# Performance work log

Hardware: AMD Instinct MI355X
Metric: run time of the kernel (lower is better)

The kernel has to match this reference:

```python
import jax, jax.numpy as jnp
import numpy as np

B, C, D, T = 64, 512, 32, 32
DT = D * T
K = 128            # valid_num: top-K proposals kept for NMS-style pooling
MARGIN = 0.2       # opt.global_margin
MAX_VIOLATION = True
EPS = 1e-8         # torch.cosine_similarity eps


def _l2n(x, axis):
    # torch cosine_similarity normalizes each vector by max(||x||, eps)
    return x / jnp.maximum(jnp.linalg.norm(x, axis=axis, keepdims=True), EPS)


def _cos(a, b, axis):
    return jnp.sum(_l2n(a, axis) * _l2n(b, axis), axis=axis)


def setup_inputs() -> dict:
    key = jax.random.key(0)
    k1, k2, k3 = jax.random.split(key, 3)
    videos = jax.random.normal(k1, (B, C, D, T), jnp.float32)
    sentences = jax.random.normal(k2, (B, C), jnp.float32)
    iou = jax.random.uniform(k3, (DT, DT), jnp.float32)
    iou_maps = 0.5 * (iou + iou.T)
    iou_maps = iou_maps.at[jnp.arange(DT), jnp.arange(DT)].set(1.0)
    mask = jnp.ones((D, T), jnp.float32)
    lam = jnp.asarray(0.125, jnp.float32)
    return {"videos": videos, "sentences": sentences, "lam": lam,
            "mask": mask, "valid_num": K, "iou_maps": iou_maps}


def reference(videos, sentences, lam, mask, valid_num, iou_maps):
    b, c, d, t = videos.shape
    dt = d * t
    # center over channel dim (dim=1 in torch)
    V = videos - jnp.mean(videos, axis=1, keepdims=True)          # [b,c,d,t]
    S = sentences - jnp.mean(sentences, axis=1, keepdims=True)    # [b,c]
    Vf = V.reshape(b, c, dt)
    Vn = _l2n(Vf, axis=1)                                         # unit over c
    Sn = _l2n(S, axis=1)
    mflat = mask.reshape(dt)

    # cosine sim of every sentence vs every video proposal: [b_sent, b_vid, dt]
    cross = jnp.einsum('ic,jcp->ijp', Sn, Vn)
    cross = jnp.where(mflat == 0, -jnp.inf, cross)

    # --- per-sample positive pooling (loop 1) ---
    self_score = cross[jnp.arange(b), jnp.arange(b)]              # [b, dt]
    w = jax.nn.softmax(self_score, axis=-1)
    video_pos = jnp.einsum('bp,bcp->bc', w, Vf)                   # [b, c]

    # sentence-sentence sims + hard negative mining
    sim = Sn @ Sn.T                                               # [b, b]
    idx = jnp.argsort(-sim, axis=1)                               # descending
    neg_idx = idx[:, 6:b - 5]                                     # b > 11 path
    neg_sents = S[neg_idx]                                        # [b, b-11, c]
    pos_score = _cos(video_pos, S, axis=1)                        # [b]
    neg_score = _cos(video_pos[:, None, :], neg_sents, axis=2)    # [b, b-11]
    vas_loss = jnp.mean(jax.nn.relu(MARGIN + neg_score - pos_score[:, None]), axis=1).mean()

    # cross-video pseudo-positive (crov), gated on nearest-neighbor sim > 0.9
    nn_idx = idx[:, 1]
    pse = Vf[nn_idx]                                              # [b, c, dt]
    vsim = jax.nn.softmax(_cos(video_pos[:, :, None], pse, axis=1), axis=-1)  # [b, dt]
    p_v = jnp.einsum('bp,bcp->bc', vsim, pse)
    n_v = jnp.einsum('bp,bcp->bc', (1.0 - vsim) * mflat, pse) / (valid_num - 1)
    crov = jax.nn.relu(MARGIN + _cos(video_pos, n_v, axis=1) - _cos(video_pos, p_v, axis=1))
    gate = sim[jnp.arange(b), nn_idx] > 0.9
    crov_loss = jnp.where(gate, crov, 0.0).mean()

    # --- NMS-weighted video score pooling (loop 2) ---
    pmap = self_score.reshape(b, d, t)                            # postive_map
    topv, topi = jax.lax.top_k(cross, valid_num)                  # [b,b,K]
    # pairwise IoU among the top-K proposals of each (sentence, video) pair
    iou = iou_maps[topi[..., :, None], topi[..., None, :]]        # [b,b,K,K]
    lower = jnp.tril(jnp.ones((valid_num, valid_num), bool), -1)  # l < k
    decay = jnp.prod(1.0 - jnp.where(lower, iou, 0.0), axis=-1)   # [b,b,K]
    wk = jax.nn.softmax(lam * topv, axis=-1)
    scores = jnp.sum(wk * decay * topv, axis=-1)                  # [b,b]

    # bidirectional margin ranking loss
    diag = jnp.diag(scores)[:, None]
    eye = jnp.eye(b, dtype=bool)
    cost_s = jnp.where(eye, 0.0, jax.nn.relu(MARGIN + scores - diag))
    cost_im = jnp.where(eye, 0.0, jax.nn.relu(MARGIN + scores - diag.T))
    if MAX_VIOLATION:
        cost_s = cost_s.max(axis=1)
        cost_im = cost_im.max(axis=0)
    loss = cost_s.sum() / b + cost_im.sum() / b + vas_loss + crov_loss
    return loss, pmap
```

## Files before the change

kernel.cpp:

```cpp
#include <hip/hip_runtime.h>
#include <hip/hip_fp16.h>
#include <math.h>

#define BB 64
#define CC 512
#define DTT 1024
#define NNEG 53
#define MARGIN_ 0.2f
#define EPSV 1e-8f
#define LDB 132

typedef short s16x8 __attribute__((ext_vector_type(8)));
typedef float f32x4 __attribute__((ext_vector_type(4)));

__device__ __forceinline__ float bred_sum(float v, float* red, int tid, int nt) {
  red[tid] = v; __syncthreads();
  for (int s = nt >> 1; s > 0; s >>= 1) { if (tid < s) red[tid] += red[tid + s]; __syncthreads(); }
  float r = red[0]; __syncthreads();
  return r;
}
__device__ __forceinline__ float bred_max(float v, float* red, int tid, int nt) {
  red[tid] = v; __syncthreads();
  for (int s = nt >> 1; s > 0; s >>= 1) { if (tid < s) red[tid] = fmaxf(red[tid], red[tid + s]); __syncthreads(); }
  float r = red[0]; __syncthreads();
  return r;
}

__global__ void k_sent(const float* __restrict__ sent, float* __restrict__ Sn,
                       float* __restrict__ SnT,
                       unsigned short* __restrict__ SnH, unsigned short* __restrict__ SnL,
                       float* __restrict__ SnSum) {
  int b = blockIdx.x, tid = threadIdx.x;
  __shared__ float red[256];
  float x0 = sent[b * CC + tid], x1 = sent[b * CC + tid + 256];
  float mean = bred_sum(x0 + x1, red, tid, 256) * (1.0f / CC);
  float s0 = x0 - mean, s1 = x1 - mean;
  float ss = bred_sum(s0 * s0 + s1 * s1, red, tid, 256);
  float nrm = fmaxf(sqrtf(ss), EPSV);
  float n0 = s0 / nrm, n1 = s1 / nrm;
  Sn[b * CC + tid] = n0; Sn[b * CC + tid + 256] = n1;
  SnT[tid * BB + b] = n0; SnT[(tid + 256) * BB + b] = n1;
  unsigned u0 = __float_as_uint(n0), u1 = __float_as_uint(n1);
  SnH[b * CC + tid] = (unsigned short)(u0 >> 16);
  SnH[b * CC + tid + 256] = (unsigned short)(u1 >> 16);
  float l0 = n0 - __uint_as_float(u0 & 0xFFFF0000u);
  float l1 = n1 - __uint_as_float(u1 & 0xFFFF0000u);
  SnL[b * CC + tid] = (unsigned short)(__float_as_uint(l0) >> 16);
  SnL[b * CC + tid + 256] = (unsigned short)(__float_as_uint(l1) >> 16);
  float sn = bred_sum(n0 + n1, red, tid, 256);
  if (tid == 0) SnSum[b] = sn;
}

__global__ void k_sim(const float* __restrict__ Sn, const float* __restrict__ SnT,
                      int* __restrict__ nn_idx, int* __restrict__ negidx,
                      float* __restrict__ nnsim) {
  int i = blockIdx.x, tid = threadIdx.x;
  int j = tid & 63, cq = tid >> 6;
  __shared__ float part[4][68];
  __shared__ float srow[BB];
  float acc = 0.f;
  const float* si = Sn + i * CC + cq * 128;
  const float* st = SnT + (size_t)(cq * 128) * BB + j;
#pragma unroll 8
  for (int c = 0; c < 128; ++c) acc = fmaf(si[c], st[(size_t)c * BB], acc);
  part[cq][j] = acc;
  __syncthreads();
  if (tid < 64) srow[tid] = part[0][tid] + part[1][tid] + part[2][tid] + part[3][tid];
  __syncthreads();
  if (tid < 64) {
    float mv = srow[tid];
    int rank = 0;
    for (int k = 0; k < BB; ++k) {
      float vk = srow[k];
      if (vk > mv || (vk == mv && k < tid)) rank++;
    }
    if (rank == 1) { nn_idx[i] = tid; nnsim[i] = mv; }
    if (rank >= 6 && rank < 59) negidx[i * NNEG + rank - 6] = tid;
  }
}

__global__ void k_prep_iou(const float* __restrict__ iou, __half* __restrict__ L16) {
  int g = (blockIdx.x * 256 + threadIdx.x) * 4;
  float4 x = *(const float4*)(iou + g);
  __half2 h0 = __floats2half2_rn(1.f - x.x, 1.f - x.y);
  __half2 h1 = __floats2half2_rn(1.f - x.z, 1.f - x.w);
  *(__half2*)(L16 + g) = h0;
  *(__half2*)(L16 + g + 2) = h1;
}

__global__ __launch_bounds__(256) void k_cross(const float* __restrict__ videos,
    const unsigned short* __restrict__ SnH, const unsigned short* __restrict__ SnL,
    const float* __restrict__ SnSum, const float* __restrict__ mask,
    float* __restrict__ cross, float* __restrict__ meanv, float* __restrict__ normv) {
  __shared__ unsigned int BH[2][16][LDB];
  __shared__ unsigned int BL[2][16][LDB];
  __shared__ float SnSum_s[64];
  __shared__ float mb_s[128];
  __shared__ float inv_s[128];

  int tid = threadIdx.x;
  int j = blockIdx.x >> 3;
  int p0 = (blockIdx.x & 7) << 7;
  int lane = tid & 63;
  int wv = tid >> 6;
  int row = lane & 15;
  int g = lane >> 4;
  int g8 = g << 3;
  int pA = wv << 5;

  int kp = tid >> 4;
  int pb = (tid & 15) << 3;

  const float* vbase = videos + ((size_t)j * CC) * DTT + p0;

  f32x4 acc[4][2];
#pragma unroll
  for (int a = 0; a < 4; ++a)
#pragma unroll
    for (int pf = 0; pf < 2; ++pf)
#pragma unroll
      for (int r = 0; r < 4; ++r) acc[a][pf][r] = 0.f;

  float sacc[8], ssacc[8];
#pragma unroll
  for (int q = 0; q < 8; ++q) { sacc[q] = 0.f; ssacc[q] = 0.f; }

  const float* pr = vbase + (size_t)(2 * kp) * DTT + pb;
  float4 f0 = *(const float4*)(pr);
  float4 f1 = *(const float4*)(pr + 4);
  float4 f2 = *(const float4*)(pr + DTT);
  float4 f3 = *(const float4*)(pr + DTT + 4);

#pragma unroll
  for (int t = 0; t < 16; ++t) {
    int kc = t * 32;
    int cb = t & 1;
    s16x8 AH[4], AL[4];
#pragma unroll
    for (int a = 0; a < 4; ++a) {
      int off = (a * 16 + row) * CC + kc + g8;
      AH[a] = *(const s16x8*)(SnH + off);
      AL[a] = *(const s16x8*)(SnL + off);
    }
    {
      float xe[8] = {f0.x, f0.y, f0.z, f0.w, f1.x, f1.y, f1.z, f1.w};
      float xo[8] = {f2.x, f2.y, f2.z, f2.w, f3.x, f3.y, f3.z, f3.w};
      unsigned int hw[8], lw[8];
#pragma unroll
      for (int q = 0; q < 8; ++q) {
        unsigned ue = __float_as_uint(xe[q]);
        unsigned uo = __float_as_uint(xo[q]);
        hw[q] = (ue >> 16) | (uo & 0xFFFF0000u);
        float el = xe[q] - __uint_as_float(ue & 0xFFFF0000u);
        float ol = xo[q] - __uint_as_float(uo & 0xFFFF0000u);
        lw[q] = (__float_as_uint(el) >> 16) | (__float_as_uint(ol) & 0xFFFF0000u);
        sacc[q] += xe[q] + xo[q];
        ssacc[q] = fmaf(xe[q], xe[q], ssacc[q]);
        ssacc[q] = fmaf(xo[q], xo[q], ssacc[q]);
      }
      *(uint4*)&BH[cb][kp][pb]     = make_uint4(hw[0], hw[1], hw[2], hw[3]);
      *(uint4*)&BH[cb][kp][pb + 4] = make_uint4(hw[4], hw[5], hw[6], hw[7]);
      *(uint4*)&BL[cb][kp][pb]     = make_uint4(lw[0], lw[1], lw[2], lw[3]);
      *(uint4*)&BL[cb][kp][pb + 4] = make_uint4(lw[4], lw[5], lw[6], lw[7]);
    }
    if (t + 1 < 16) {
      const float* pn = vbase + (size_t)((t + 1) * 32 + 2 * kp) * DTT + pb;
      f0 = *(const float4*)(pn);
      f1 = *(const float4*)(pn + 4);
      f2 = *(const float4*)(pn + DTT);
      f3 = *(const float4*)(pn + DTT + 4);
    }
    __syncthreads();
#pragma unroll
    for (int pf = 0; pf < 2; ++pf) {
      int p = pA + pf * 16 + row;
      int kpb = g << 2;
      union { unsigned int u[4]; s16x8 v; } bh, bl;
      bh.u[0] = BH[cb][kpb][p]; bh.u[1] = BH[cb][kpb + 1][p];
      bh.u[2] = BH[cb][kpb + 2][p]; bh.u[3] = BH[cb][kpb + 3][p];
      bl.u[0] = BL[cb][kpb][p]; bl.u[1] = BL[cb][kpb + 1][p];
      bl.u[2] = BL[cb][kpb + 2][p]; bl.u[3] = BL[cb][kpb + 3][p];
#pragma unroll
      for (int a = 0; a < 4; ++a) {
        acc[a][pf] = __builtin_amdgcn_mfma_f32_16x16x32_bf16(AH[a], bh.v, acc[a][pf], 0, 0, 0);
        acc[a][pf] = __builtin_amdgcn_mfma_f32_16x16x32_bf16(AH[a], bl.v, acc[a][pf], 0, 0, 0);
        acc[a][pf] = __builtin_amdgcn_mfma_f32_16x16x32_bf16(AL[a], bh.v, acc[a][pf], 0, 0, 0);
      }
    }
  }

  float (*Sred)[LDB] = (float(*)[LDB])&BH[0][0][0];
  float (*SSred)[LDB] = (float(*)[LDB])&BL[0][0][0];
#pragma unroll
  for (int q = 0; q < 8; ++q) { Sred[kp][pb + q] = sacc[q]; SSred[kp][pb + q] = ssacc[q]; }
  if (tid < 64) SnSum_s[tid] = SnSum[tid];
  __syncthreads();
  if (tid < 128) {
    float s = 0.f, ss = 0.f;
#pragma unroll
    for (int k = 0; k < 16; ++k) { s += Sred[k][tid]; ss += SSred[k][tid]; }
    float mb = s * (1.0f / CC);
    float var = ss - s * mb;
    float nrm = fmaxf(sqrtf(fmaxf(var, 0.f)), EPSV);
    meanv[j * DTT + p0 + tid] = mb;
    normv[j * DTT + p0 + tid] = nrm;
    mb_s[tid] = mb;
    inv_s[tid] = 1.f / nrm;
  }
  __syncthreads();

#pragma unroll
  for (int pf = 0; pf < 2; ++pf) {
    int p = pA + pf * 16 + row;
    float mb = mb_s[p], inv = inv_s[p];
    float mk = mask[p0 + p];
#pragma unroll
    for (int a = 0; a < 4; ++a) {
#pragma unroll
      for (int r = 0; r < 4; ++r) {
        int i = a * 16 + (g << 2) + r;
        float val = (acc[a][pf][r] - mb * SnSum_s[i]) * inv;
        if (mk == 0.f) val = -INFINITY;
        cross[((size_t)i * BB + j) * DTT + p0 + p] = val;
      }
    }
  }
}

__global__ void k_softmax_w(const float* __restrict__ cross, const float* __restrict__ meanv,
                            float* __restrict__ pmap, float* __restrict__ w, float* __restrict__ wm) {
  int b = blockIdx.x, tid = threadIdx.x;
  __shared__ float red[256];
  const float* row = cross + ((size_t)b * BB + b) * DTT;
  float v[4]; float mx = -INFINITY;
#pragma unroll
  for (int q = 0; q < 4; ++q) {
    v[q] = row[q * 256 + tid];
    pmap[b * DTT + q * 256 + tid] = v[q];
    mx = fmaxf(mx, v[q]);
  }
  mx = bred_max(mx, red, tid, 256);
  float e[4]; float se = 0.f;
#pragma unroll
  for (int q = 0; q < 4; ++q) { e[q] = expf(v[q] - mx); se += e[q]; }
  se = bred_sum(se, red, tid, 256);
  float inv = 1.f / se;
  float wmacc = 0.f;
#pragma unroll
  for (int q = 0; q < 4; ++q) {
    float wv = e[q] * inv;
    w[b * DTT + q * 256 + tid] = wv;
    wmacc += wv * meanv[b * DTT + q * 256 + tid];
  }
  wmacc = bred_sum(wmacc, red, tid, 256);
  if (tid == 0) wm[b] = wmacc;
}

__global__ void k_vpos(const float* __restrict__ videos, const float* __restrict__ w,
                       const float* __restrict__ wm, float* __restrict__ vp) {
  int wid = (blockIdx.x * 256 + threadIdx.x) >> 6;
  int lane = threadIdx.x & 63;
  int b = wid >> 9, c = wid & 511;
  const float4* vb = (const float4*)(videos + (size_t)(b * CC + c) * DTT) + lane * 4;
  const float4* wb = (const float4*)(w + b * DTT) + lane * 4;
  float acc = 0.f;
#pragma unroll
  for (int q = 0; q < 4; ++q) {
    float4 x = vb[q], y = wb[q];
    acc += x.x * y.x + x.y * y.y + x.z * y.z + x.w * y.w;
  }
#pragma unroll
  for (int off = 32; off > 0; off >>= 1) acc += __shfl_xor(acc, off);
  if (lane == 0) vp[b * CC + c] = acc - wm[b];
}

__global__ void k_vpnorm(const float* __restrict__ vp, float* __restrict__ vpn,
                         float* __restrict__ vpsum) {
  int b = blockIdx.x, tid = threadIdx.x;
  __shared__ float red[256];
  float x0 = vp[b * CC + tid], x1 = vp[b * CC + tid + 256];
  float ss = bred_sum(x0 * x0 + x1 * x1, red, tid, 256);
  float sm = bred_sum(x0 + x1, red, tid, 256);
  if (tid == 0) { vpn[b] = fmaxf(sqrtf(ss), EPSV); vpsum[b] = sm; }
}

__global__ void k_vsim_logits(const float* __restrict__ videos, const float* __restrict__ vp,
    const float* __restrict__ vpn, const float* __restrict__ vpsum, const int* __restrict__ nn_idx,
    const float* __restrict__ meanv, const float* __restrict__ normv, float* __restrict__ vslog) {
  int gid = blockIdx.x * 256 + threadIdx.x;
  int b = gid >> 10, p = gid & 1023;
  int nn = nn_idx[b];
  const float* base = videos + (size_t)nn * CC * DTT + p;
  const float* vpr = vp + b * CC;
  float acc = 0.f;
#pragma unroll 1
  for (int c0 = 0; c0 < CC; c0 += 16) {
    float v[16];
#pragma unroll
    for (int u = 0; u < 16; ++u) v[u] = base[(size_t)(c0 + u) * DTT];
#pragma unroll
    for (int u = 0; u < 16; ++u) acc = fmaf(vpr[c0 + u], v[u], acc);
  }
  acc -= meanv[nn * DTT + p] * vpsum[b];
  vslog[gid] = acc / (vpn[b] * normv[nn * DTT + p]);
}

__global__ void k_softmax_vsim(float* __restrict__ vslog, const int* __restrict__ nn_idx,
    const float* __restrict__ meanv, const float* __restrict__ mask,
    float* __restrict__ svp, float* __restrict__ svn) {
  int b = blockIdx.x, tid = threadIdx.x;
  __shared__ float red[256];
  int nn = nn_idx[b];
  float v[4]; float mx = -INFINITY;
#pragma unroll
  for (int q = 0; q < 4; ++q) { v[q] = vslog[b * DTT + q * 256 + tid]; mx = fmaxf(mx, v[q]); }
  mx = bred_max(mx, red, tid, 256);
  float e[4]; float se = 0.f;
#pragma unroll
  for (int q = 0; q < 4; ++q) { e[q] = expf(v[q] - mx); se += e[q]; }
  se = bred_sum(se, red, tid, 256);
  float inv = 1.f / se;
  float sp = 0.f, sn2 = 0.f;
#pragma unroll
  for (int q = 0; q < 4; ++q) {
    int p = q * 256 + tid;
    float vs = e[q] * inv;
    vslog[b * DTT + p] = vs;
    float mm = meanv[nn * DTT + p];
    sp += vs * mm;
    sn2 += (1.f - vs) * mask[p] * mm;
  }
  sp = bred_sum(sp, red, tid, 256);
  sn2 = bred_sum(sn2, red, tid, 256);
  if (tid == 0) { svp[b] = sp; svn[b] = sn2; }
}

__global__ void k_pvnv(const float* __restrict__ videos, const float* __restrict__ vsim,
    const int* __restrict__ nn_idx, const float* __restrict__ mask,
    const float* __restrict__ svp, const float* __restrict__ svn, const int* __restrict__ vn_p,
    float* __restrict__ pv, float* __restrict__ nv) {
  int wid = (blockIdx.x * 256 + threadIdx.x) >> 6;
  int lane = threadIdx.x & 63;
  int b = wid >> 9, c = wid & 511;
  int nn = nn_idx[b];
  const float4* vb = (const float4*)(videos + (size_t)(nn * CC + c) * DTT) + lane * 4;
  const float4* vs4 = (const float4*)(vsim + b * DTT) + lane * 4;
  const float4* m4 = ((const float4*)mask) + lane * 4;
  float ap = 0.f, an = 0.f;
#pragma unroll
  for (int q = 0; q < 4; ++q) {
    float4 x = vb[q], s = vs4[q], m = m4[q];
    ap += x.x * s.x + x.y * s.y + x.z * s.z + x.w * s.w;
    an += x.x * (1.f - s.x) * m.x + x.y * (1.f - s.y) * m.y + x.z * (1.f - s.z) * m.z + x.w * (1.f - s.w) * m.w;
  }
#pragma unroll
  for (int off = 32; off > 0; off >>= 1) { ap += __shfl_xor(ap, off); an += __shfl_xor(an, off); }
  if (lane == 0) {
    float kd = (float)(*vn_p - 1);
    pv[b * CC + c] = ap - svp[b];
    nv[b * CC + c] = (an - svn[b]) / kd;
  }
}

__global__ void k_vas(const float* __restrict__ vp, const float* __restrict__ vpn,
                      const float* __restrict__ SnT, const int* __restrict__ negidx,
                      float* __restrict__ vasrow) {
  int i = blockIdx.x, tid = threadIdx.x;
  int t = tid & 63, cq = tid >> 6;
  __shared__ float part[4][68];
  __shared__ float redv[64];
  __shared__ float red[256];
  int nj = (t < NNEG) ? negidx[i * NNEG + t] : i;
  float acc = 0.f;
  const float* vpr = vp + i * CC + cq * 128;
  const float* st = SnT + (size_t)(cq * 128) * BB + nj;
#pragma unroll 8
  for (int c = 0; c < 128; ++c) acc = fmaf(vpr[c], st[(size_t)c * BB], acc);
  part[cq][t] = acc;
  __syncthreads();
  if (tid < 64) redv[tid] = part[0][tid] + part[1][tid] + part[2][tid] + part[3][tid];
  __syncthreads();
  float invn = 1.f / vpn[i];
  float pos = redv[63] * invn;
  float contrib = (tid < NNEG) ? fmaxf(MARGIN_ + redv[tid] * invn - pos, 0.f) : 0.f;
  float s = bred_sum(contrib, red, tid, 256);
  if (tid == 0) vasrow[i] = s / (float)NNEG;
}

__global__ void k_crov(const float* __restrict__ vp, const float* __restrict__ vpn,
                       const float* __restrict__ pv, const float* __restrict__ nv,
                       const float* __restrict__ nnsim, float* __restrict__ crovrow) {
  int b = blockIdx.x, tid = threadIdx.x;
  __shared__ float red[256];
  float dp = 0.f, pp = 0.f, dn = 0.f, nn2 = 0.f;
  for (int c = tid; c < CC; c += 256) {
    float a = vp[b * CC + c], x = pv[b * CC + c], y = nv[b * CC + c];
    dp += a * x; pp += x * x; dn += a * y; nn2 += y * y;
  }
  dp = bred_sum(dp, red, tid, 256);
  pp = bred_sum(pp, red, tid, 256);
  dn = bred_sum(dn, red, tid, 256);
  nn2 = bred_sum(nn2, red, tid, 256);
  if (tid == 0) {
    float cosp = dp / (vpn[b] * fmaxf(sqrtf(pp), EPSV));
    float cosn = dn / (vpn[b] * fmaxf(sqrtf(nn2), EPSV));
    float crov = fmaxf(MARGIN_ + cosn - cosp, 0.f);
    crovrow[b] = (nnsim[b] > 0.9f) ? crov : 0.f;
  }
}

__global__ __launch_bounds__(256) void k_select(const float* __restrict__ cross,
    const int* __restrict__ vn_p, unsigned* __restrict__ ordi_g, float* __restrict__ ordv_g) {
  __shared__ unsigned int hist_s[4][256];
  __shared__ unsigned int sel_s[4][128];
  __shared__ unsigned int selk_s[4][128];
  __shared__ unsigned int cnt_s[4];
  int tid = threadIdx.x;
  int wv = tid >> 6, lane = tid & 63;
  int ij = blockIdx.x * 4 + wv;
  int K = *vn_p; if (K > 128) K = 128;
  unsigned int* hist = hist_s[wv];
  unsigned int* sel = sel_s[wv];
  unsigned int* selk = selk_s[wv];

  const float* row = cross + (size_t)ij * DTT;
  unsigned int v[16];
#pragma unroll
  for (int q = 0; q < 16; ++q) {
    unsigned u = __float_as_uint(row[q * 64 + lane]);
    v[q] = (u & 0x80000000u) ? ~u : (u | 0x80000000u);
  }
  if (lane == 0) cnt_s[wv] = 0u;
  __builtin_amdgcn_wave_barrier();

  unsigned prefix = 0u, pmask = 0u;
  int remaining = K;
  for (int shift = 24; shift >= 0; shift -= 8) {
#pragma unroll
    for (int q = 0; q < 4; ++q) hist[lane * 4 + q] = 0u;
    __builtin_amdgcn_wave_barrier();
#pragma unroll
    for (int q = 0; q < 16; ++q) {
      if ((v[q] & pmask) == prefix)
        atomicAdd(&hist[(v[q] >> shift) & 255u], 1u);
    }
    __builtin_amdgcn_wave_barrier();
    unsigned c0 = hist[lane * 4], c1 = hist[lane * 4 + 1];
    unsigned c2 = hist[lane * 4 + 2], c3 = hist[lane * 4 + 3];
    unsigned s = c0 + c1 + c2 + c3;
    unsigned inc = s;
#pragma unroll
    for (int off = 1; off < 64; off <<= 1) {
      unsigned t = __shfl_down(inc, off);
      if (lane + off < 64) inc += t;
    }
    unsigned exc = inc - s;
    bool found = (exc < (unsigned)remaining) && (inc >= (unsigned)remaining);
    unsigned long long bmask = __ballot(found);
    int winner = (int)(__ffsll((unsigned long long)bmask) - 1);
    unsigned packed = 0u;
    if (found) {
      unsigned c = exc;
      unsigned cc[4] = {c0, c1, c2, c3};
      int d = lane * 4;
#pragma unroll
      for (int q = 3; q >= 0; --q) {
        if (c + cc[q] >= (unsigned)remaining) { d = lane * 4 + q; break; }
        c += cc[q];
      }
      packed = ((unsigned)d << 16) | (unsigned)(remaining - (int)c);
    }
    packed = __shfl(packed, winner);
    prefix |= (packed >> 16) << shift;
    remaining = (int)(packed & 0xFFFFu);
    pmask |= 255u << shift;
  }

#pragma unroll
  for (int q = 0; q < 16; ++q) {
    if (v[q] > prefix) {
      unsigned pos = atomicAdd(&cnt_s[wv], 1u);
      sel[pos] = (unsigned)(q * 64 + lane);
      selk[pos] = v[q];
    }
  }
  __builtin_amdgcn_wave_barrier();
  {
    int base = K - remaining;
    int last = -1;
    for (int t = 0; t < remaining; ++t) {
      int mymin = 0x7FFFFFFF;
#pragma unroll
      for (int q = 0; q < 16; ++q) {
        int idx = q * 64 + lane;
        if (v[q] == prefix && idx > last && idx < mymin) mymin = idx;
      }
#pragma unroll
      for (int off = 32; off > 0; off >>= 1) mymin = min(mymin, __shfl_xor(mymin, off));
      if (lane == 0) { sel[base + t] = (unsigned)mymin; selk[base + t] = prefix; }
      last = mymin;
    }
  }
  __builtin_amdgcn_wave_barrier();

  for (int e = lane; e < K; e += 64) {
    unsigned myidx = sel[e], myk = selk[e];
    int rank = 0;
    for (int m = 0; m < K; ++m) {
      unsigned ok = selk[m];
      rank += (ok > myk || (ok == myk && sel[m] < myidx)) ? 1 : 0;
    }
    unsigned u = (myk & 0x80000000u) ? (myk & 0x7FFFFFFFu) : ~myk;
    ordi_g[ij * 128 + rank] = myidx;
    ordv_g[ij * 128 + rank] = __uint_as_float(u);
  }
}

__global__ __launch_bounds__(256) void k_decay(const __half* __restrict__ L16,
    const unsigned* __restrict__ ordi_g, const float* __restrict__ ordv_g,
    const float* __restrict__ lam_p, const int* __restrict__ vn_p,
    float* __restrict__ scores) {
  __shared__ unsigned ti[128];
  __shared__ float dks[128];
  int ij = blockIdx.x, tid = threadIdx.x;
  int wv = tid >> 6, lane = tid & 63;
  int K = *vn_p; if (K > 128) K = 128;
  float lam = *lam_p;
  if (tid < 128) {
    ti[tid] = (tid < K) ? ordi_g[ij * 128 + tid] : 0u;
    dks[tid] = 1.f;
  }
  __syncthreads();

  for (int r = wv; r < K; r += 4) {
    const __half* irow = L16 + (size_t)ti[r] * DTT;
    float f = 1.f;
    if (lane < r && lane < 64) f = __half2float(irow[ti[lane]]);
    float prod = f;
#pragma unroll
    for (int off = 32; off > 0; off >>= 1) prod *= __shfl_xor(prod, off);
    if (r > 64 && prod > 1e-14f) {
      float f2 = 1.f;
      int m = 64 + lane;
      if (m < r) f2 = __half2float(irow[ti[m]]);
#pragma unroll
      for (int off = 32; off > 0; off >>= 1) f2 *= __shfl_xor(f2, off);
      prod *= f2;
    }
    if (lane == 0) dks[r] = prod;
  }
  __syncthreads();

  if (wv == 0) {
    bool okA = (lane < K), okB = (lane + 64 < K);
    float vA = okA ? ordv_g[ij * 128 + lane] : 0.f;
    float vB = okB ? ordv_g[ij * 128 + lane + 64] : 0.f;
    float mx = fmaxf(okA ? lam * vA : -INFINITY, okB ? lam * vB : -INFINITY);
#pragma unroll
    for (int off = 32; off > 0; off >>= 1) mx = fmaxf(mx, __shfl_xor(mx, off));
    float eA = okA ? expf(lam * vA - mx) : 0.f;
    float eB = okB ? expf(lam * vB - mx) : 0.f;
    float se = eA + eB;
    float sc = (okA ? eA * dks[lane] * vA : 0.f) + (okB ? eB * dks[lane + 64] * vB : 0.f);
#pragma unroll
    for (int off = 32; off > 0; off >>= 1) {
      se += __shfl_xor(se, off);
      sc += __shfl_xor(sc, off);
    }
    if (lane == 0) scores[ij] = sc / se;
  }
}

__global__ void k_final(const float* __restrict__ scores, const float* __restrict__ vasrow,
                        const float* __restrict__ crovrow, float* __restrict__ out) {
  int tid = threadIdx.x;
  __shared__ float sm[BB * BB];
  __shared__ float red[64];
  for (int q = tid; q < BB * BB; q += 64) sm[q] = scores[q];
  __syncthreads();
  float di = sm[tid * BB + tid];
  float rowmax = 0.f, colmax = 0.f;
  for (int k = 0; k < BB; ++k) {
    if (k != tid) {
      rowmax = fmaxf(rowmax, fmaxf(MARGIN_ + sm[tid * BB + k] - di, 0.f));
      colmax = fmaxf(colmax, fmaxf(MARGIN_ + sm[k * BB + tid] - di, 0.f));
    }
  }
  float total = bred_sum(rowmax + colmax + vasrow[tid] + crovrow[tid], red, tid, 64);
  if (tid == 0) out[0] = total * (1.0f / BB);
}

extern "C" void kernel_launch(void* const* d_in, const int* in_sizes, int n_in,
                              void* d_out, int out_size, void* d_ws, size_t ws_size,
                              hipStream_t stream) {
  const float* videos = (const float*)d_in[0];
  const float* sentences = (const float*)d_in[1];
  const float* lam = (const float*)d_in[2];
  const float* mask = (const float*)d_in[3];
  const int* valid_num = (const int*)d_in[4];
  const float* iou_maps = (const float*)d_in[5];
  float* out = (float*)d_out;
  float* pmap = out + 1;

  float* ws = (float*)d_ws;
  float* Sn = ws;
  float* SnT = Sn + 32768;
  float* SnSum = SnT + 32768;
  float* meanv = SnSum + 64;
  float* normv = meanv + 65536;
  float* cross = normv + 65536;
  float* w = cross + 4194304;
  float* wm = w + 65536;
  float* vp = wm + 64;
  float* vpn = vp + 32768;
  float* vpsum = vpn + 64;
  float* nnsim = vpsum + 64;
  float* vslog = nnsim + 64;
  float* svp = vslog + 65536;
  float* svn = svp + 64;
  float* pvb = svn + 64;
  float* nvb = pvb + 32768;
  float* vasrow = nvb + 32768;
  float* crovrow = vasrow + 64;
  float* scores = crovrow + 64;
  int* nn_idx = (int*)(scores + 4096);
  int* negidx = nn_idx + 64;
  unsigned* ordi_g = (unsigned*)(negidx + 3392);
  float* ordv_g = (float*)(ordi_g + 524288);
  __half* L16 = (__half*)(ordv_g + 524288);
  unsigned short* SnH16 = (unsigned short*)(L16 + 1048576);
  unsigned short* SnL16 = SnH16 + 32768;

  k_sent<<<64, 256, 0, stream>>>(sentences, Sn, SnT, SnH16, SnL16, SnSum);
  k_sim<<<64, 256, 0, stream>>>(Sn, SnT, nn_idx, negidx, nnsim);
  k_prep_iou<<<1024, 256, 0, stream>>>(iou_maps, L16);
  k_cross<<<512, 256, 0, stream>>>(videos, SnH16, SnL16, SnSum, mask, cross, meanv, normv);
  k_softmax_w<<<64, 256, 0, stream>>>(cross, meanv, pmap, w, wm);
  k_vpos<<<8192, 256, 0, stream>>>(videos, w, wm, vp);
  k_vpnorm<<<64, 256, 0, stream>>>(vp, vpn, vpsum);
  k_vsim_logits<<<256, 256, 0, stream>>>(videos, vp, vpn, vpsum, nn_idx, meanv, normv, vslog);
  k_softmax_vsim<<<64, 256, 0, stream>>>(vslog, nn_idx, meanv, mask, svp, svn);
  k_pvnv<<<8192, 256, 0, stream>>>(videos, vslog, nn_idx, mask, svp, svn, valid_num, pvb, nvb);
  k_vas<<<64, 256, 0, stream>>>(vp, vpn, SnT, negidx, vasrow);
  k_crov<<<64, 256, 0, stream>>>(vp, vpn, pvb, nvb, nnsim, crovrow);
  k_select<<<1024, 256, 0, stream>>>(cross, valid_num, ordi_g, ordv_g);
  k_decay<<<4096, 256, 0, stream>>>(L16, ordi_g, ordv_g, lam, valid_num, scores);
  k_final<<<1, 64, 0, stream>>>(scores, vasrow, crovrow, out);
}
```

Baseline: 417.5 us.

## Fuse small kernels and merge top-K select into decay kernel

```diff
diff --git a/kernel.cpp b/kernel.cpp
--- a/kernel.cpp
+++ b/kernel.cpp
@@ -26,11 +26,21 @@
   return r;
 }
 
-__global__ void k_sent(const float* __restrict__ sent, float* __restrict__ Sn,
-                       float* __restrict__ SnT,
-                       unsigned short* __restrict__ SnH, unsigned short* __restrict__ SnL,
-                       float* __restrict__ SnSum) {
-  int b = blockIdx.x, tid = threadIdx.x;
+__global__ void k_sentprep(const float* __restrict__ sent, const float* __restrict__ iou,
+                           float* __restrict__ Sn, float* __restrict__ SnT,
+                           unsigned short* __restrict__ SnH, unsigned short* __restrict__ SnL,
+                           float* __restrict__ SnSum, __half* __restrict__ L16) {
+  int tid = threadIdx.x;
+  if (blockIdx.x >= 64) {
+    int g = ((blockIdx.x - 64) * 256 + tid) * 4;
+    float4 x = *(const float4*)(iou + g);
+    __half2 h0 = __floats2half2_rn(1.f - x.x, 1.f - x.y);
+    __half2 h1 = __floats2half2_rn(1.f - x.z, 1.f - x.w);
+    *(__half2*)(L16 + g) = h0;
+    *(__half2*)(L16 + g + 2) = h1;
+    return;
+  }
+  int b = blockIdx.x;
   __shared__ float red[256];
   float x0 = sent[b * CC + tid], x1 = sent[b * CC + tid + 256];
   float mean = bred_sum(x0 + x1, red, tid, 256) * (1.0f / CC);
@@ -79,15 +89,6 @@
   }
 }
 
-__global__ void k_prep_iou(const float* __restrict__ iou, __half* __restrict__ L16) {
-  int g = (blockIdx.x * 256 + threadIdx.x) * 4;
-  float4 x = *(const float4*)(iou + g);
-  __half2 h0 = __floats2half2_rn(1.f - x.x, 1.f - x.y);
-  __half2 h1 = __floats2half2_rn(1.f - x.z, 1.f - x.w);
-  *(__half2*)(L16 + g) = h0;
-  *(__half2*)(L16 + g + 2) = h1;
-}
-
 __global__ __launch_bounds__(256) void k_cross(const float* __restrict__ videos,
     const unsigned short* __restrict__ SnH, const unsigned short* __restrict__ SnL,
     const float* __restrict__ SnSum, const float* __restrict__ mask,
@@ -228,9 +229,11 @@
 }
 
 __global__ void k_softmax_w(const float* __restrict__ cross, const float* __restrict__ meanv,
-                            float* __restrict__ pmap, float* __restrict__ w, float* __restrict__ wm) {
+                            float* __restrict__ pmap, float* __restrict__ w, float* __restrict__ wm,
+                            float* __restrict__ vpsum_a, float* __restrict__ vpss_a) {
   int b = blockIdx.x, tid = threadIdx.x;
   __shared__ float red[256];
+  if (tid == 0) { vpsum_a[b] = 0.f; vpss_a[b] = 0.f; }
   const float* row = cross + ((size_t)b * BB + b) * DTT;
   float v[4]; float mx = -INFINITY;
 #pragma unroll
@@ -257,7 +260,8 @@
 }
 
 __global__ void k_vpos(const float* __restrict__ videos, const float* __restrict__ w,
-                       const float* __restrict__ wm, float* __restrict__ vp) {
+                       const float* __restrict__ wm, float* __restrict__ vp,
+                       float* __restrict__ vpsum_a, float* __restrict__ vpss_a) {
   int wid = (blockIdx.x * 256 + threadIdx.x) >> 6;
   int lane = threadIdx.x & 63;
   int b = wid >> 9, c = wid & 511;
@@ -271,21 +275,16 @@
   }
 #pragma unroll
   for (int off = 32; off > 0; off >>= 1) acc += __shfl_xor(acc, off);
-  if (lane == 0) vp[b * CC + c] = acc - wm[b];
-}
-
-__global__ void k_vpnorm(const float* __restrict__ vp, float* __restrict__ vpn,
-                         float* __restrict__ vpsum) {
-  int b = blockIdx.x, tid = threadIdx.x;
-  __shared__ float red[256];
-  float x0 = vp[b * CC + tid], x1 = vp[b * CC + tid + 256];
-  float ss = bred_sum(x0 * x0 + x1 * x1, red, tid, 256);
-  float sm = bred_sum(x0 + x1, red, tid, 256);
-  if (tid == 0) { vpn[b] = fmaxf(sqrtf(ss), EPSV); vpsum[b] = sm; }
+  if (lane == 0) {
+    float val = acc - wm[b];
+    vp[b * CC + c] = val;
+    atomicAdd(&vpsum_a[b], val);
+    atomicAdd(&vpss_a[b], val * val);
+  }
 }
 
 __global__ void k_vsim_logits(const float* __restrict__ videos, const float* __restrict__ vp,
-    const float* __restrict__ vpn, const float* __restrict__ vpsum, const int* __restrict__ nn_idx,
+    const float* __restrict__ vpss_a, const float* __restrict__ vpsum_a, const int* __restrict__ nn_idx,
     const float* __restrict__ meanv, const float* __restrict__ normv, float* __restrict__ vslog) {
   int gid = blockIdx.x * 256 + threadIdx.x;
   int b = gid >> 10, p = gid & 1023;
@@ -301,8 +300,9 @@
 #pragma unroll
     for (int u = 0; u < 16; ++u) acc = fmaf(vpr[c0 + u], v[u], acc);
   }
-  acc -= meanv[nn * DTT + p] * vpsum[b];
-  vslog[gid] = acc / (vpn[b] * normv[nn * DTT + p]);
+  acc -= meanv[nn * DTT + p] * vpsum_a[b];
+  float vpn = fmaxf(sqrtf(vpss_a[b]), EPSV);
+  vslog[gid] = acc / (vpn * normv[nn * DTT + p]);
 }
 
 __global__ void k_softmax_vsim(float* __restrict__ vslog, const int* __restrict__ nn_idx,
@@ -362,173 +362,159 @@
   }
 }
 
-__global__ void k_vas(const float* __restrict__ vp, const float* __restrict__ vpn,
-                      const float* __restrict__ SnT, const int* __restrict__ negidx,
-                      float* __restrict__ vasrow) {
+__global__ void k_vascrov(const float* __restrict__ vp, const float* __restrict__ vpss_a,
+                          const float* __restrict__ SnT, const int* __restrict__ negidx,
+                          const float* __restrict__ pv, const float* __restrict__ nv,
+                          const float* __restrict__ nnsim,
+                          float* __restrict__ vasrow, float* __restrict__ crovrow) {
   int i = blockIdx.x, tid = threadIdx.x;
   int t = tid & 63, cq = tid >> 6;
   __shared__ float part[4][68];
   __shared__ float redv[64];
   __shared__ float red[256];
-  int nj = (t < NNEG) ? negidx[i * NNEG + t] : i;
-  float acc = 0.f;
-  const float* vpr = vp + i * CC + cq * 128;
-  const float* st = SnT + (size_t)(cq * 128) * BB + nj;
+  float invn = 1.f / fmaxf(sqrtf(vpss_a[i]), EPSV);
+  {
+    int nj = (t < NNEG) ? negidx[i * NNEG + t] : i;
+    float acc = 0.f;
+    const float* vpr = vp + i * CC + cq * 128;
+    const float* st = SnT + (size_t)(cq * 128) * BB + nj;
 #pragma unroll 8
-  for (int c = 0; c < 128; ++c) acc = fmaf(vpr[c], st[(size_t)c * BB], acc);
-  part[cq][t] = acc;
-  __syncthreads();
-  if (tid < 64) redv[tid] = part[0][tid] + part[1][tid] + part[2][tid] + part[3][tid];
-  __syncthreads();
-  float invn = 1.f / vpn[i];
-  float pos = redv[63] * invn;
-  float contrib = (tid < NNEG) ? fmaxf(MARGIN_ + redv[tid] * invn - pos, 0.f) : 0.f;
-  float s = bred_sum(contrib, red, tid, 256);
-  if (tid == 0) vasrow[i] = s / (float)NNEG;
-}
-
-__global__ void k_crov(const float* __restrict__ vp, const float* __restrict__ vpn,
-                       const float* __restrict__ pv, const float* __restrict__ nv,
-                       const float* __restrict__ nnsim, float* __restrict__ crovrow) {
-  int b = blockIdx.x, tid = threadIdx.x;
-  __shared__ float red[256];
-  float dp = 0.f, pp = 0.f, dn = 0.f, nn2 = 0.f;
-  for (int c = tid; c < CC; c += 256) {
-    float a = vp[b * CC + c], x = pv[b * CC + c], y = nv[b * CC + c];
-    dp += a * x; pp += x * x; dn += a * y; nn2 += y * y;
-  }
-  dp = bred_sum(dp, red, tid, 256);
-  pp = bred_sum(pp, red, tid, 256);
-  dn = bred_sum(dn, red, tid, 256);
-  nn2 = bred_sum(nn2, red, tid, 256);
-  if (tid == 0) {
-    float cosp = dp / (vpn[b] * fmaxf(sqrtf(pp), EPSV));
-    float cosn = dn / (vpn[b] * fmaxf(sqrtf(nn2), EPSV));
-    float crov = fmaxf(MARGIN_ + cosn - cosp, 0.f);
-    crovrow[b] = (nnsim[b] > 0.9f) ? crov : 0.f;
-  }
-}
-
-__global__ __launch_bounds__(256) void k_select(const float* __restrict__ cross,
-    const int* __restrict__ vn_p, unsigned* __restrict__ ordi_g, float* __restrict__ ordv_g) {
-  __shared__ unsigned int hist_s[4][256];
-  __shared__ unsigned int sel_s[4][128];
-  __shared__ unsigned int selk_s[4][128];
-  __shared__ unsigned int cnt_s[4];
-  int tid = threadIdx.x;
-  int wv = tid >> 6, lane = tid & 63;
-  int ij = blockIdx.x * 4 + wv;
-  int K = *vn_p; if (K > 128) K = 128;
-  unsigned int* hist = hist_s[wv];
-  unsigned int* sel = sel_s[wv];
-  unsigned int* selk = selk_s[wv];
-
-  const float* row = cross + (size_t)ij * DTT;
-  unsigned int v[16];
-#pragma unroll
-  for (int q = 0; q < 16; ++q) {
-    unsigned u = __float_as_uint(row[q * 64 + lane]);
-    v[q] = (u & 0x80000000u) ? ~u : (u | 0x80000000u);
-  }
-  if (lane == 0) cnt_s[wv] = 0u;
-  __builtin_amdgcn_wave_barrier();
-
-  unsigned prefix = 0u, pmask = 0u;
-  int remaining = K;
-  for (int shift = 24; shift >= 0; shift -= 8) {
-#pragma unroll
-    for (int q = 0; q < 4; ++q) hist[lane * 4 + q] = 0u;
-    __builtin_amdgcn_wave_barrier();
-#pragma unroll
-    for (int q = 0; q < 16; ++q) {
-      if ((v[q] & pmask) == prefix)
-        atomicAdd(&hist[(v[q] >> shift) & 255u], 1u);
-    }
-    __builtin_amdgcn_wave_barrier();
-    unsigned c0 = hist[lane * 4], c1 = hist[lane * 4 + 1];
-    unsigned c2 = hist[lane * 4 + 2], c3 = hist[lane * 4 + 3];
-    unsigned s = c0 + c1 + c2 + c3;
-    unsigned inc = s;
-#pragma unroll
-    for (int off = 1; off < 64; off <<= 1) {
-      unsigned t = __shfl_down(inc, off);
-      if (lane + off < 64) inc += t;
-    }
-    unsigned exc = inc - s;
-    bool found = (exc < (unsigned)remaining) && (inc >= (unsigned)remaining);
-    unsigned long long bmask = __ballot(found);
-    int winner = (int)(__ffsll((unsigned long long)bmask) - 1);
-    unsigned packed = 0u;
-    if (found) {
-      unsigned c = exc;
-      unsigned cc[4] = {c0, c1, c2, c3};
-      int d = lane * 4;
-#pragma unroll
-      for (int q = 3; q >= 0; --q) {
-        if (c + cc[q] >= (unsigned)remaining) { d = lane * 4 + q; break; }
-        c += cc[q];
-      }
-      packed = ((unsigned)d << 16) | (unsigned)(remaining - (int)c);
-    }
-    packed = __shfl(packed, winner);
-    prefix |= (packed >> 16) << shift;
-    remaining = (int)(packed & 0xFFFFu);
-    pmask |= 255u << shift;
-  }
-
-#pragma unroll
-  for (int q = 0; q < 16; ++q) {
-    if (v[q] > prefix) {
-      unsigned pos = atomicAdd(&cnt_s[wv], 1u);
-      sel[pos] = (unsigned)(q * 64 + lane);
-      selk[pos] = v[q];
-    }
-  }
-  __builtin_amdgcn_wave_barrier();
+    for (int c = 0; c < 128; ++c) acc = fmaf(vpr[c], st[(size_t)c * BB], acc);
+    part[cq][t] = acc;
+    __syncthreads();
+    if (tid < 64) redv[tid] = part[0][tid] + part[1][tid] + part[2][tid] + part[3][tid];
+    __syncthreads();
+    float pos = redv[63] * invn;
+    float contrib = (tid < NNEG) ? fmaxf(MARGIN_ + redv[tid] * invn - pos, 0.f) : 0.f;
+    float s = bred_sum(contrib, red, tid, 256);
+    if (tid == 0) vasrow[i] = s / (float)NNEG;
+  }
   {
-    int base = K - remaining;
-    int last = -1;
-    for (int t = 0; t < remaining; ++t) {
-      int mymin = 0x7FFFFFFF;
-#pragma unroll
-      for (int q = 0; q < 16; ++q) {
-        int idx = q * 64 + lane;
-        if (v[q] == prefix && idx > last && idx < mymin) mymin = idx;
-      }
-#pragma unroll
-      for (int off = 32; off > 0; off >>= 1) mymin = min(mymin, __shfl_xor(mymin, off));
-      if (lane == 0) { sel[base + t] = (unsigned)mymin; selk[base + t] = prefix; }
-      last = mymin;
-    }
-  }
-  __builtin_amdgcn_wave_barrier();
-
-  for (int e = lane; e < K; e += 64) {
-    unsigned myidx = sel[e], myk = selk[e];
-    int rank = 0;
-    for (int m = 0; m < K; ++m) {
-      unsigned ok = selk[m];
-      rank += (ok > myk || (ok == myk && sel[m] < myidx)) ? 1 : 0;
-    }
-    unsigned u = (myk & 0x80000000u) ? (myk & 0x7FFFFFFFu) : ~myk;
-    ordi_g[ij * 128 + rank] = myidx;
-    ordv_g[ij * 128 + rank] = __uint_as_float(u);
-  }
-}
-
-__global__ __launch_bounds__(256) void k_decay(const __half* __restrict__ L16,
-    const unsigned* __restrict__ ordi_g, const float* __restrict__ ordv_g,
-    const float* __restrict__ lam_p, const int* __restrict__ vn_p,
-    float* __restrict__ scores) {
+    float dp = 0.f, pp = 0.f, dn = 0.f, nn2 = 0.f;
+    for (int c = tid; c < CC; c += 256) {
+      float a = vp[i * CC + c], x = pv[i * CC + c], y = nv[i * CC + c];
+      dp += a * x; pp += x * x; dn += a * y; nn2 += y * y;
+    }
+    dp = bred_sum(dp, red, tid, 256);
+    pp = bred_sum(pp, red, tid, 256);
+    dn = bred_sum(dn, red, tid, 256);
+    nn2 = bred_sum(nn2, red, tid, 256);
+    if (tid == 0) {
+      float cosp = dp * invn / fmaxf(sqrtf(pp), EPSV);
+      float cosn = dn * invn / fmaxf(sqrtf(nn2), EPSV);
+      float crov = fmaxf(MARGIN_ + cosn - cosp, 0.f);
+      crovrow[i] = (nnsim[i] > 0.9f) ? crov : 0.f;
+    }
+  }
+}
+
+__global__ __launch_bounds__(256) void k_seldecay(const float* __restrict__ cross,
+    const __half* __restrict__ L16, const float* __restrict__ lam_p,
+    const int* __restrict__ vn_p, float* __restrict__ scores) {
+  __shared__ unsigned int hist[256];
+  __shared__ unsigned int sel[128];
+  __shared__ unsigned int selk[128];
+  __shared__ unsigned int cnt;
   __shared__ unsigned ti[128];
+  __shared__ float tv[128];
   __shared__ float dks[128];
   int ij = blockIdx.x, tid = threadIdx.x;
   int wv = tid >> 6, lane = tid & 63;
   int K = *vn_p; if (K > 128) K = 128;
   float lam = *lam_p;
-  if (tid < 128) {
-    ti[tid] = (tid < K) ? ordi_g[ij * 128 + tid] : 0u;
-    dks[tid] = 1.f;
+
+  if (wv == 0) {
+    const float* row = cross + (size_t)ij * DTT;
+    unsigned int v[16];
+#pragma unroll
+    for (int q = 0; q < 16; ++q) {
+      unsigned u = __float_as_uint(row[q * 64 + lane]);
+      v[q] = (u & 0x80000000u) ? ~u : (u | 0x80000000u);
+    }
+    if (lane == 0) cnt = 0u;
+    __builtin_amdgcn_wave_barrier();
+
+    unsigned prefix = 0u, pmask = 0u;
+    int remaining = K;
+    for (int shift = 24; shift >= 0; shift -= 8) {
+#pragma unroll
+      for (int q = 0; q < 4; ++q) hist[lane * 4 + q] = 0u;
+      __builtin_amdgcn_wave_barrier();
+#pragma unroll
+      for (int q = 0; q < 16; ++q) {
+        if ((v[q] & pmask) == prefix)
+          atomicAdd(&hist[(v[q] >> shift) & 255u], 1u);
+      }
+      __builtin_amdgcn_wave_barrier();
+      unsigned c0 = hist[lane * 4], c1 = hist[lane * 4 + 1];
+      unsigned c2 = hist[lane * 4 + 2], c3 = hist[lane * 4 + 3];
+      unsigned s = c0 + c1 + c2 + c3;
+      unsigned inc = s;
+#pragma unroll
+      for (int off = 1; off < 64; off <<= 1) {
+        unsigned t = __shfl_down(inc, off);
+        if (lane + off < 64) inc += t;
+      }
+      unsigned exc = inc - s;
+      bool found = (exc < (unsigned)remaining) && (inc >= (unsigned)remaining);
+      unsigned long long bmask = __ballot(found);
+      int winner = (int)(__ffsll((unsigned long long)bmask) - 1);
+      unsigned packed = 0u;
+      if (found) {
+        unsigned c = exc;
+        unsigned cc[4] = {c0, c1, c2, c3};
+        int d = lane * 4;
+#pragma unroll
+        for (int q = 3; q >= 0; --q) {
+          if (c + cc[q] >= (unsigned)remaining) { d = lane * 4 + q; break; }
+          c += cc[q];
+        }
+        packed = ((unsigned)d << 16) | (unsigned)(remaining - (int)c);
+      }
+      packed = __shfl(packed, winner);
+      prefix |= (packed >> 16) << shift;
+      remaining = (int)(packed & 0xFFFFu);
+      pmask |= 255u << shift;
+    }
+
+#pragma unroll
+    for (int q = 0; q < 16; ++q) {
+      if (v[q] > prefix) {
+        unsigned pos = atomicAdd(&cnt, 1u);
+        sel[pos] = (unsigned)(q * 64 + lane);
+        selk[pos] = v[q];
+      }
+    }
+    __builtin_amdgcn_wave_barrier();
+    {
+      int base = K - remaining;
+      int last = -1;
+      for (int t = 0; t < remaining; ++t) {
+        int mymin = 0x7FFFFFFF;
+#pragma unroll
+        for (int q = 0; q < 16; ++q) {
+          int idx = q * 64 + lane;
+          if (v[q] == prefix && idx > last && idx < mymin) mymin = idx;
+        }
+#pragma unroll
+        for (int off = 32; off > 0; off >>= 1) mymin = min(mymin, __shfl_xor(mymin, off));
+        if (lane == 0) { sel[base + t] = (unsigned)mymin; selk[base + t] = prefix; }
+        last = mymin;
+      }
+    }
+    __builtin_amdgcn_wave_barrier();
+
+    for (int e = lane; e < K; e += 64) {
+      unsigned myidx = sel[e], myk = selk[e];
+      int rank = 0;
+      for (int m = 0; m < K; ++m) {
+        unsigned ok = selk[m];
+        rank += (ok > myk || (ok == myk && sel[m] < myidx)) ? 1 : 0;
+      }
+      unsigned u = (myk & 0x80000000u) ? (myk & 0x7FFFFFFFu) : ~myk;
+      ti[rank] = myidx;
+      tv[rank] = __uint_as_float(u);
+    }
   }
   __syncthreads();
 
@@ -553,8 +539,8 @@
 
   if (wv == 0) {
     bool okA = (lane < K), okB = (lane + 64 < K);
-    float vA = okA ? ordv_g[ij * 128 + lane] : 0.f;
-    float vB = okB ? ordv_g[ij * 128 + lane + 64] : 0.f;
+    float vA = okA ? tv[lane] : 0.f;
+    float vB = okB ? tv[lane + 64] : 0.f;
     float mx = fmaxf(okA ? lam * vA : -INFINITY, okB ? lam * vB : -INFINITY);
 #pragma unroll
     for (int off = 32; off > 0; off >>= 1) mx = fmaxf(mx, __shfl_xor(mx, off));
@@ -612,9 +598,9 @@
   float* w = cross + 4194304;
   float* wm = w + 65536;
   float* vp = wm + 64;
-  float* vpn = vp + 32768;
-  float* vpsum = vpn + 64;
-  float* nnsim = vpsum + 64;
+  float* vpss_a = vp + 32768;
+  float* vpsum_a = vpss_a + 64;
+  float* nnsim = vpsum_a + 64;
   float* vslog = nnsim + 64;
   float* svp = vslog + 65536;
   float* svn = svp + 64;
@@ -625,25 +611,21 @@
   float* scores = crovrow + 64;
   int* nn_idx = (int*)(scores + 4096);
   int* negidx = nn_idx + 64;
-  unsigned* ordi_g = (unsigned*)(negidx + 3392);
-  float* ordv_g = (float*)(ordi_g + 524288);
-  __half* L16 = (__half*)(ordv_g + 524288);
+  unsigned* ordi_unused = (unsigned*)(negidx + 3392);
+  float* ordv_unused = (float*)(ordi_unused + 524288);
+  __half* L16 = (__half*)(ordv_unused + 524288);
   unsigned short* SnH16 = (unsigned short*)(L16 + 1048576);
   unsigned short* SnL16 = SnH16 + 32768;
 
-  k_sent<<<64, 256, 0, stream>>>(sentences, Sn, SnT, SnH16, SnL16, SnSum);
+  k_sentprep<<<1088, 256, 0, stream>>>(sentences, iou_maps, Sn, SnT, SnH16, SnL16, SnSum, L16);
   k_sim<<<64, 256, 0, stream>>>(Sn, SnT, nn_idx, negidx, nnsim);
-  k_prep_iou<<<1024, 256, 0, stream>>>(iou_maps, L16);
   k_cross<<<512, 256, 0, stream>>>(videos, SnH16, SnL16, SnSum, mask, cross, meanv, normv);
-  k_softmax_w<<<64, 256, 0, stream>>>(cross, meanv, pmap, w, wm);
-  k_vpos<<<8192, 256, 0, stream>>>(videos, w, wm, vp);
-  k_vpnorm<<<64, 256, 0, stream>>>(vp, vpn, vpsum);
-  k_vsim_logits<<<256, 256, 0, stream>>>(videos, vp, vpn, vpsum, nn_idx, meanv, normv, vslog);
+  k_softmax_w<<<64, 256, 0, stream>>>(cross, meanv, pmap, w, wm, vpsum_a, vpss_a);
+  k_vpos<<<8192, 256, 0, stream>>>(videos, w, wm, vp, vpsum_a, vpss_a);
+  k_vsim_logits<<<256, 256, 0, stream>>>(videos, vp, vpss_a, vpsum_a, nn_idx, meanv, normv, vslog);
   k_softmax_vsim<<<64, 256, 0, stream>>>(vslog, nn_idx, meanv, mask, svp, svn);
   k_pvnv<<<8192, 256, 0, stream>>>(videos, vslog, nn_idx, mask, svp, svn, valid_num, pvb, nvb);
-  k_vas<<<64, 256, 0, stream>>>(vp, vpn, SnT, negidx, vasrow);
-  k_crov<<<64, 256, 0, stream>>>(vp, vpn, pvb, nvb, nnsim, crovrow);
-  k_select<<<1024, 256, 0, stream>>>(cross, valid_num, ordi_g, ordv_g);
-  k_decay<<<4096, 256, 0, stream>>>(L16, ordi_g, ordv_g, lam, valid_num, scores);
+  k_vascrov<<<64, 256, 0, stream>>>(vp, vpss_a, SnT, negidx, pvb, nvb, nnsim, vasrow, crovrow);
+  k_seldecay<<<4096, 256, 0, stream>>>(cross, L16, lam, valid_num, scores);
   k_final<<<1, 64, 0, stream>>>(scores, vasrow, crovrow, out);
 }
```

Result: slower. 670.9 us (+60.7%).
